# Kernel tuning notes

Hardware: AMD Instinct MI355X
Metric: run time of the kernel (lower is better)

## Reference

```python
import jax, jax.numpy as jnp
import numpy as np

B, N, D = 1024, 100000, 512


def setup_inputs() -> dict:
    key = jax.random.key(0)
    k1, k2, k3 = jax.random.split(key, 3)
    x_t = jax.random.normal(k1, (B, D), dtype=jnp.float32)
    # keep t away from 0/1 so b_t = 1 - t is well conditioned
    t = jax.random.uniform(k2, (B,), dtype=jnp.float32, minval=0.05, maxval=0.95)
    dataset = jax.random.normal(k3, (N, D), dtype=jnp.float32)
    return {"x_t": x_t, "t": t, "dataset": dataset}


def reference(x_t, t, dataset):
    # Straight-line AffineInterp: a_t = t, b_t = 1 - t, dot_a = 1, dot_b = -1.
    # Original detaches coeffs (detach=True).
    a_t = jax.lax.stop_gradient(t)
    b_t = jax.lax.stop_gradient(1.0 - t)
    dot_a_t = jnp.ones_like(a_t)
    dot_b_t = -jnp.ones_like(b_t)

    dataset_norm = jnp.sum(dataset * dataset, axis=1)          # (N,)
    term_1 = jnp.sum(x_t * x_t, axis=1)                        # (B,)
    term_2 = jnp.einsum('bd,nd->bn', x_t, dataset)             # (B, N)

    # ||x_t - a_t * x1||^2 expanded, scaled by -1/(2 b_t^2)
    logit = (term_1[:, None]
             - 2.0 * a_t[:, None] * term_2
             + (a_t * a_t)[:, None] * dataset_norm[None, :])
    logit = (-1.0 / (2.0 * b_t * b_t))[:, None] * logit        # (B, N)

    prob = jax.nn.softmax(logit, axis=1)                       # (B, N)
    data_coeff = dot_a_t - a_t * dot_b_t / b_t                 # (B,)
    prob = prob * data_coeff[:, None]

    weighted_dataset = jnp.einsum('bn,nd->bd', prob, dataset)  # (B, D)
    v = (dot_b_t / b_t)[:, None] * x_t + weighted_dataset
    return v
```

## Files before the change

### kernel.cpp

```cpp
#include <hip/hip_runtime.h>
#include <math.h>

#define B_SZ 1024
#define N_SZ 100000
#define D_SZ 512
#define NBLK 3125

typedef __attribute__((ext_vector_type(8))) short short8;
typedef __attribute__((ext_vector_type(16))) float float16;

__device__ __forceinline__ unsigned f2bf(float x) {
    unsigned u = __float_as_uint(x);
    u += 0x7FFFu + ((u >> 16) & 1u);
    return u >> 16;
}
__device__ __forceinline__ float bf2f(unsigned h) {
    return __uint_as_float(h << 16);
}

__global__ __launch_bounds__(256) void pre_kernel(
    const float* __restrict__ ds, const float* __restrict__ x_t,
    short* __restrict__ Yh, short* __restrict__ Yl, short* __restrict__ Yt,
    short* __restrict__ Xh, short* __restrict__ Xl, float* __restrict__ norms)
{
    __shared__ unsigned short YS[32 * 512];
    const int bx = blockIdx.x, tid = threadIdx.x;
    if (bx < NBLK) {
        const int row = tid >> 3, seg = tid & 7;
        const size_t g = (size_t)(bx * 32 + row) * 512 + seg * 64;
        const int ls = row * 512 + seg * 64;
        float nrm = 0.f;
        #pragma unroll
        for (int i = 0; i < 16; i++) {
            float4 v = *(const float4*)(ds + g + i * 4);
            nrm += v.x*v.x + v.y*v.y + v.z*v.z + v.w*v.w;
            unsigned h0 = f2bf(v.x), h1 = f2bf(v.y), h2 = f2bf(v.z), h3 = f2bf(v.w);
            unsigned l0 = f2bf(v.x - bf2f(h0)), l1 = f2bf(v.y - bf2f(h1));
            unsigned l2 = f2bf(v.z - bf2f(h2)), l3 = f2bf(v.w - bf2f(h3));
            uint2 hw = make_uint2(h0 | (h1 << 16), h2 | (h3 << 16));
            uint2 lw = make_uint2(l0 | (l1 << 16), l2 | (l3 << 16));
            *(uint2*)(Yh + g + i * 4) = hw;
            *(uint2*)(Yl + g + i * 4) = lw;
            *(uint2*)(YS + ls + i * 4) = hw;
        }
        nrm += __shfl_xor(nrm, 1, 64);
        nrm += __shfl_xor(nrm, 2, 64);
        nrm += __shfl_xor(nrm, 4, 64);
        if ((tid & 7) == 0) norms[bx * 32 + row] = nrm;
        __syncthreads();
        #pragma unroll
        for (int r = 0; r < 2; r++) {
            const int d = tid + r * 256;
            unsigned w[16];
            #pragma unroll
            for (int j = 0; j < 16; j++) {
                unsigned lo = YS[(2 * j) * 512 + d];
                unsigned hi = YS[(2 * j + 1) * 512 + d];
                w[j] = lo | (hi << 16);
            }
            uint4* dst = (uint4*)(Yt + (size_t)bx * 16384 + d * 32);
            dst[0] = make_uint4(w[0], w[1], w[2], w[3]);
            dst[1] = make_uint4(w[4], w[5], w[6], w[7]);
            dst[2] = make_uint4(w[8], w[9], w[10], w[11]);
            dst[3] = make_uint4(w[12], w[13], w[14], w[15]);
        }
    } else {
        const int xb = bx - NBLK;
        #pragma unroll
        for (int k = 0; k < 16; k++) {
            const size_t i4 = (size_t)xb * 4096 + k * 256 + tid;
            float4 v = *(const float4*)(x_t + i4 * 4);
            unsigned h0 = f2bf(v.x), h1 = f2bf(v.y), h2 = f2bf(v.z), h3 = f2bf(v.w);
            unsigned l0 = f2bf(v.x - bf2f(h0)), l1 = f2bf(v.y - bf2f(h1));
            unsigned l2 = f2bf(v.z - bf2f(h2)), l3 = f2bf(v.w - bf2f(h3));
            *(uint2*)(Xh + i4 * 4) = make_uint2(h0 | (h1 << 16), h2 | (h3 << 16));
            *(uint2*)(Xl + i4 * 4) = make_uint2(l0 | (l1 << 16), l2 | (l3 << 16));
        }
    }
}

__global__ __launch_bounds__(512, 2) void attn_kernel(
    const float* __restrict__ t,
    const short* __restrict__ Xh, const short* __restrict__ Xl,
    const short* __restrict__ Yh, const short* __restrict__ Yl,
    const short* __restrict__ Yt, const float* __restrict__ norms,
    float* __restrict__ m_part, float* __restrict__ l_part,
    float* __restrict__ acc_part, int chunk)
{
    __shared__ short YhL[2 * 32 * 512];
    __shared__ float slots[4 * 64 * 33];
    __shared__ float Pbuf[64 * 36];
    __shared__ float c1A[64], c2A[64], mAs[64], lAs[64], alA[64];
    __shared__ float nrmL[32];

    const int tid = threadIdx.x;
    const int wave = tid >> 6, lane = tid & 63;
    const int half = lane >> 5, l31 = lane & 31;

    int qbi = blockIdx.x, si = blockIdx.y;
    if (gridDim.x == 16 && (gridDim.y & 7) == 0) {
        int g = gridDim.y >> 3;
        int fid = blockIdx.x + blockIdx.y * 16;
        int xcd = fid & 7, j = fid >> 3;
        si = xcd + 8 * (j % g);
        qbi = j / g;
    }
    const int qb = qbi * 64;
    const int s = si;
    const int n0s = s * chunk;
    const int n1 = min(N_SZ, n0s + chunk);
    const int numTiles = (n1 - n0s + 31) >> 5;

    if (tid < 64) {
        float tv = t[qb + tid];
        float bt = 1.0f - tv;
        float i2 = 1.0f / (2.0f * bt * bt);
        c1A[tid] = 2.0f * tv * i2;
        c2A[tid] = tv * tv * i2;
        mAs[tid] = -1e30f;
        lAs[tid] = 0.0f;
        alA[tid] = 0.0f;
    }

    if (wave < 4) {
        short8 XF[2][8][2];
        #pragma unroll
        for (int qt = 0; qt < 2; qt++)
            #pragma unroll
            for (int kc = 0; kc < 8; kc++) {
                size_t off = (size_t)(qb + qt * 32 + l31) * 512 + wave * 128 + kc * 16 + half * 8;
                XF[qt][kc][0] = *(const short8*)(Xh + off);
                XF[qt][kc][1] = *(const short8*)(Xl + off);
            }
        {
            #pragma unroll
            for (int j = 0; j < 8; j++) {
                int r = wave * 8 + j;
                const int gsw = (lane * 8) ^ ((r & 7) << 3);
                const short* gh = Yh + (size_t)(n0s + r) * 512 + gsw;
                __builtin_amdgcn_global_load_lds(
                    (const __attribute__((address_space(1))) unsigned int*)gh,
                    (__attribute__((address_space(3))) unsigned int*)&YhL[r * 512], 16, 0, 0);
            }
        }
        __syncthreads();

        for (int it = 0; it <= numTiles; ++it) {
            short8 ALf[8];
            if (it < numTiles) {
                const int n0 = n0s + it * 32;
                const short* ylrow = Yl + (size_t)(n0 + l31) * 512 + wave * 128 + half * 8;
                #pragma unroll
                for (int kc = 0; kc < 8; kc++)
                    ALf[kc] = *(const short8*)(ylrow + kc * 16);
                if (wave == 0 && lane < 32) nrmL[lane] = norms[n0 + lane];
            }
            if (it + 1 < numTiles) {
                const int n0n = n0s + (it + 1) * 32;
                short* dstb = YhL + ((it + 1) & 1) * (32 * 512);
                #pragma unroll
                for (int j = 0; j < 8; j++) {
                    int r = wave * 8 + j;
                    const int gsw = (lane * 8) ^ ((r & 7) << 3);
                    const short* gh = Yh + (size_t)(n0n + r) * 512 + gsw;
                    __builtin_amdgcn_global_load_lds(
                        (const __attribute__((address_space(1))) unsigned int*)gh,
                        (__attribute__((address_space(3))) unsigned int*)&dstb[r * 512], 16, 0, 0);
                }
            }
            if (it < numTiles) {
                const short* Yb = YhL + (it & 1) * (32 * 512);
                float16 S0, S1;
                #pragma unroll
                for (int e = 0; e < 16; e++) { S0[e] = 0.f; S1[e] = 0.f; }
                #pragma unroll
                for (int kc = 0; kc < 8; kc++) {
                    const int koff = wave * 128 + kc * 16 + half * 8;
                    const int ksw = koff ^ ((l31 & 7) << 3);
                    short8 Ah = *(const short8*)(Yb + l31 * 512 + ksw);
                    S0 = __builtin_amdgcn_mfma_f32_32x32x16_bf16(Ah, XF[0][kc][0], S0, 0, 0, 0);
                    S0 = __builtin_amdgcn_mfma_f32_32x32x16_bf16(Ah, XF[0][kc][1], S0, 0, 0, 0);
                    S0 = __builtin_amdgcn_mfma_f32_32x32x16_bf16(ALf[kc], XF[0][kc][0], S0, 0, 0, 0);
                    S1 = __builtin_amdgcn_mfma_f32_32x32x16_bf16(Ah, XF[1][kc][0], S1, 0, 0, 0);
                    S1 = __builtin_amdgcn_mfma_f32_32x32x16_bf16(Ah, XF[1][kc][1], S1, 0, 0, 0);
                    S1 = __builtin_amdgcn_mfma_f32_32x32x16_bf16(ALf[kc], XF[1][kc][0], S1, 0, 0, 0);
                }
                float* sb = &slots[wave * 2112];
                #pragma unroll
                for (int qt = 0; qt < 2; qt++) {
                    float* rowp = sb + (qt * 32 + l31) * 33;
                    #pragma unroll
                    for (int r = 0; r < 16; r++) {
                        int n = (r & 3) + 8 * (r >> 2) + 4 * half;
                        rowp[n] = qt ? S1[r] : S0[r];
                    }
                }
            }
            __syncthreads();

            if (it < numTiles) {
                int ql = lane >> 2, nq = lane & 3;
                int q = wave * 16 + ql;
                float c1q = c1A[q], c2q = c2A[q];
                float lg[8];
                float mt = -1e30f;
                #pragma unroll
                for (int j = 0; j < 8; j++) {
                    int n = nq * 8 + j;
                    float dd = slots[q * 33 + n] + slots[2112 + q * 33 + n]
                             + slots[4224 + q * 33 + n] + slots[6336 + q * 33 + n];
                    lg[j] = c1q * dd - c2q * nrmL[n];
                    mt = fmaxf(mt, lg[j]);
                }
                mt = fmaxf(mt, __shfl_xor(mt, 1, 64));
                mt = fmaxf(mt, __shfl_xor(mt, 2, 64));
                float mo = mAs[q];
                float mn = fmaxf(mo, mt);
                float al = __expf(mo - mn);
                float ls = 0.f;
                #pragma unroll
                for (int j = 0; j < 8; j++) {
                    float p = __expf(lg[j] - mn);
                    Pbuf[q * 36 + nq * 8 + j] = p;
                    ls += p;
                }
                ls += __shfl_xor(ls, 1, 64);
                ls += __shfl_xor(ls, 2, 64);
                if (nq == 0) {
                    mAs[q] = mn;
                    lAs[q] = lAs[q] * al + ls;
                    alA[q] = al;
                }
            }
            __syncthreads();
        }
        if (tid < 64) {
            m_part[(size_t)s * B_SZ + qb + tid] = mAs[tid];
            l_part[(size_t)s * B_SZ + qb + tid] = lAs[tid];
        }
    } else {
        const int dbase = (wave - 4) * 128;
        float16 O[4][2];
        #pragma unroll
        for (int dt = 0; dt < 4; dt++)
            #pragma unroll
            for (int qt = 0; qt < 2; qt++)
                #pragma unroll
                for (int e = 0; e < 16; e++) O[dt][qt][e] = 0.f;

        __syncthreads();

        for (int it = 0; it <= numTiles; ++it) {
            if (it > 0) {
                int blk = (n0s + (it - 1) * 32) >> 5;
                const short* yb = Yt + (size_t)blk * 16384;
                short8 AF[4][2];
                #pragma unroll
                for (int dt = 0; dt < 4; dt++)
                    #pragma unroll
                    for (int kc = 0; kc < 2; kc++)
                        AF[dt][kc] = *(const short8*)(yb + (dbase + dt * 32 + l31) * 32 + kc * 16 + half * 8);
                float al0 = alA[l31], al1 = alA[32 + l31];
                #pragma unroll
                for (int dt = 0; dt < 4; dt++) {
                    O[dt][0] *= al0;
                    O[dt][1] *= al1;
                }
                short8 BF[2][2];
                #pragma unroll
                for (int qt = 0; qt < 2; qt++)
                    #pragma unroll
                    for (int kc = 0; kc < 2; kc++) {
                        const float* pr = &Pbuf[(qt * 32 + l31) * 36 + kc * 16 + half * 8];
                        float4 pa = *(const float4*)pr;
                        float4 pb = *(const float4*)(pr + 4);
                        short8 b;
                        b[0] = (short)f2bf(pa.x); b[1] = (short)f2bf(pa.y);
                        b[2] = (short)f2bf(pa.z); b[3] = (short)f2bf(pa.w);
                        b[4] = (short)f2bf(pb.x); b[5] = (short)f2bf(pb.y);
                        b[6] = (short)f2bf(pb.z); b[7] = (short)f2bf(pb.w);
                        BF[qt][kc] = b;
                    }
                #pragma unroll
                for (int dt = 0; dt < 4; dt++)
                    #pragma unroll
                    for (int qt = 0; qt < 2; qt++)
                        #pragma unroll
                        for (int kc = 0; kc < 2; kc++)
                            O[dt][qt] = __builtin_amdgcn_mfma_f32_32x32x16_bf16(
                                AF[dt][kc], BF[qt][kc], O[dt][qt], 0, 0, 0);
            }
            __syncthreads();
            __syncthreads();
        }
        #pragma unroll
        for (int dt = 0; dt < 4; dt++)
            #pragma unroll
            for (int qt = 0; qt < 2; qt++) {
                int q = qb + qt * 32 + l31;
                float* op = acc_part + ((size_t)s * B_SZ + q) * D_SZ + dbase + dt * 32 + 4 * half;
                #pragma unroll
                for (int rg = 0; rg < 4; rg++) {
                    float4 v = make_float4(O[dt][qt][4 * rg], O[dt][qt][4 * rg + 1],
                                           O[dt][qt][4 * rg + 2], O[dt][qt][4 * rg + 3]);
                    *(float4*)(op + 8 * rg) = v;
                }
            }
    }
}

__global__ __launch_bounds__(256) void combine_kernel(
    const float* __restrict__ x_t, const float* __restrict__ t,
    const float* __restrict__ m_part, const float* __restrict__ l_part,
    const float* __restrict__ acc_part, float* __restrict__ out, int nsplit)
{
    int q = blockIdx.x;
    int tid = threadIdx.x;
    float M = -1e30f;
    for (int s = 0; s < nsplit; s++) M = fmaxf(M, m_part[(size_t)s * B_SZ + q]);
    float L = 0.f;
    for (int s = 0; s < nsplit; s++)
        L += l_part[(size_t)s * B_SZ + q] * __expf(m_part[(size_t)s * B_SZ + q] - M);

    float tv = t[q];
    float bt = 1.0f - tv;
    float coeff = 1.0f + tv / bt;
    float invb = 1.0f / bt;
    float invL = 1.0f / L;

    int d = tid * 2;
    float2 w = make_float2(0.f, 0.f);
    for (int s = 0; s < nsplit; s++) {
        float sc = __expf(m_part[(size_t)s * B_SZ + q] - M);
        float2 av = *(const float2*)(acc_part + ((size_t)s * B_SZ + q) * D_SZ + d);
        w.x += sc * av.x; w.y += sc * av.y;
    }
    float2 xv = *(const float2*)(x_t + (size_t)q * D_SZ + d);
    float2 o;
    o.x = -invb * xv.x + coeff * w.x * invL;
    o.y = -invb * xv.y + coeff * w.y * invL;
    *(float2*)(out + (size_t)q * D_SZ + d) = o;
}

extern "C" void kernel_launch(void* const* d_in, const int* in_sizes, int n_in,
                              void* d_out, int out_size, void* d_ws, size_t ws_size,
                              hipStream_t stream) {
    const float* x_t = (const float*)d_in[0];
    const float* t   = (const float*)d_in[1];
    const float* ds  = (const float*)d_in[2];
    float* out = (float*)d_out;

    short* wsS = (short*)d_ws;
    short* Yh = wsS;
    short* Yl = wsS + 51200000;
    short* Yt = wsS + 102400000;
    short* Xh = wsS + 153600000;
    short* Xl = wsS + 154124288;
    float* fbase = (float*)((char*)d_ws + 309297152);
    float* norms = fbase;
    int nsplit = 16;
    while (nsplit > 1 &&
           309697152ULL + (size_t)nsplit * 1024 * 4 * (2 + 512) > ws_size)
        nsplit >>= 1;
    float* m_part = fbase + 100000;
    float* l_part = m_part + (size_t)nsplit * B_SZ;
    float* acc    = l_part + (size_t)nsplit * B_SZ;
    int chunk = 32 * ((N_SZ + 32 * nsplit - 1) / (32 * nsplit));

    pre_kernel<<<dim3(NBLK + 32), dim3(256), 0, stream>>>(ds, x_t, Yh, Yl, Yt, Xh, Xl, norms);
    attn_kernel<<<dim3(16, nsplit), dim3(512), 0, stream>>>(
        t, Xh, Xl, Yh, Yl, Yt, norms, m_part, l_part, acc, chunk);
    combine_kernel<<<dim3(B_SZ), dim3(256), 0, stream>>>(
        x_t, t, m_part, l_part, acc, out, nsplit);
}
```

Before: 1.218 ms.

## Stage low-bf16 dataset tile through LDS and split MFMA accumulator chains

```diff
diff --git a/kernel.cpp b/kernel.cpp
--- a/kernel.cpp
+++ b/kernel.cpp
@@ -88,6 +88,7 @@
     float* __restrict__ acc_part, int chunk)
 {
     __shared__ short YhL[2 * 32 * 512];
+    __shared__ short YlL[32 * 512];
     __shared__ float slots[4 * 64 * 33];
     __shared__ float Pbuf[64 * 36];
     __shared__ float c1A[64], c2A[64], mAs[64], lAs[64], alA[64];
@@ -132,29 +133,22 @@
                 XF[qt][kc][0] = *(const short8*)(Xh + off);
                 XF[qt][kc][1] = *(const short8*)(Xl + off);
             }
-        {
-            #pragma unroll
-            for (int j = 0; j < 8; j++) {
-                int r = wave * 8 + j;
-                const int gsw = (lane * 8) ^ ((r & 7) << 3);
-                const short* gh = Yh + (size_t)(n0s + r) * 512 + gsw;
-                __builtin_amdgcn_global_load_lds(
-                    (const __attribute__((address_space(1))) unsigned int*)gh,
-                    (__attribute__((address_space(3))) unsigned int*)&YhL[r * 512], 16, 0, 0);
-            }
+        #pragma unroll
+        for (int j = 0; j < 8; j++) {
+            int r = wave * 8 + j;
+            const int gsw = (lane * 8) ^ ((r & 7) << 3);
+            const short* gh = Yh + (size_t)(n0s + r) * 512 + gsw;
+            const short* gl = Yl + (size_t)(n0s + r) * 512 + gsw;
+            __builtin_amdgcn_global_load_lds(
+                (const __attribute__((address_space(1))) unsigned int*)gh,
+                (__attribute__((address_space(3))) unsigned int*)&YhL[r * 512], 16, 0, 0);
+            __builtin_amdgcn_global_load_lds(
+                (const __attribute__((address_space(1))) unsigned int*)gl,
+                (__attribute__((address_space(3))) unsigned int*)&YlL[r * 512], 16, 0, 0);
         }
         __syncthreads();
 
         for (int it = 0; it <= numTiles; ++it) {
-            short8 ALf[8];
-            if (it < numTiles) {
-                const int n0 = n0s + it * 32;
-                const short* ylrow = Yl + (size_t)(n0 + l31) * 512 + wave * 128 + half * 8;
-                #pragma unroll
-                for (int kc = 0; kc < 8; kc++)
-                    ALf[kc] = *(const short8*)(ylrow + kc * 16);
-                if (wave == 0 && lane < 32) nrmL[lane] = norms[n0 + lane];
-            }
             if (it + 1 < numTiles) {
                 const int n0n = n0s + (it + 1) * 32;
                 short* dstb = YhL + ((it + 1) & 1) * (32 * 512);
@@ -169,22 +163,29 @@
                 }
             }
             if (it < numTiles) {
+                if (wave == 0 && lane < 32) nrmL[lane] = norms[n0s + it * 32 + lane];
                 const short* Yb = YhL + (it & 1) * (32 * 512);
-                float16 S0, S1;
-                #pragma unroll
-                for (int e = 0; e < 16; e++) { S0[e] = 0.f; S1[e] = 0.f; }
+                float16 S0a, S0b, S0c, S1a, S1b, S1c;
+                #pragma unroll
+                for (int e = 0; e < 16; e++) {
+                    S0a[e] = 0.f; S0b[e] = 0.f; S0c[e] = 0.f;
+                    S1a[e] = 0.f; S1b[e] = 0.f; S1c[e] = 0.f;
+                }
+                __builtin_amdgcn_s_setprio(1);
                 #pragma unroll
                 for (int kc = 0; kc < 8; kc++) {
                     const int koff = wave * 128 + kc * 16 + half * 8;
                     const int ksw = koff ^ ((l31 & 7) << 3);
                     short8 Ah = *(const short8*)(Yb + l31 * 512 + ksw);
-                    S0 = __builtin_amdgcn_mfma_f32_32x32x16_bf16(Ah, XF[0][kc][0], S0, 0, 0, 0);
-                    S0 = __builtin_amdgcn_mfma_f32_32x32x16_bf16(Ah, XF[0][kc][1], S0, 0, 0, 0);
-                    S0 = __builtin_amdgcn_mfma_f32_32x32x16_bf16(ALf[kc], XF[0][kc][0], S0, 0, 0, 0);
-                    S1 = __builtin_amdgcn_mfma_f32_32x32x16_bf16(Ah, XF[1][kc][0], S1, 0, 0, 0);
-                    S1 = __builtin_amdgcn_mfma_f32_32x32x16_bf16(Ah, XF[1][kc][1], S1, 0, 0, 0);
-                    S1 = __builtin_amdgcn_mfma_f32_32x32x16_bf16(ALf[kc], XF[1][kc][0], S1, 0, 0, 0);
-                }
+                    short8 Al = *(const short8*)(YlL + l31 * 512 + ksw);
+                    S0a = __builtin_amdgcn_mfma_f32_32x32x16_bf16(Ah, XF[0][kc][0], S0a, 0, 0, 0);
+                    S0b = __builtin_amdgcn_mfma_f32_32x32x16_bf16(Ah, XF[0][kc][1], S0b, 0, 0, 0);
+                    S0c = __builtin_amdgcn_mfma_f32_32x32x16_bf16(Al, XF[0][kc][0], S0c, 0, 0, 0);
+                    S1a = __builtin_amdgcn_mfma_f32_32x32x16_bf16(Ah, XF[1][kc][0], S1a, 0, 0, 0);
+                    S1b = __builtin_amdgcn_mfma_f32_32x32x16_bf16(Ah, XF[1][kc][1], S1b, 0, 0, 0);
+                    S1c = __builtin_amdgcn_mfma_f32_32x32x16_bf16(Al, XF[1][kc][0], S1c, 0, 0, 0);
+                }
+                __builtin_amdgcn_s_setprio(0);
                 float* sb = &slots[wave * 2112];
                 #pragma unroll
                 for (int qt = 0; qt < 2; qt++) {
@@ -192,12 +193,26 @@
                     #pragma unroll
                     for (int r = 0; r < 16; r++) {
                         int n = (r & 3) + 8 * (r >> 2) + 4 * half;
-                        rowp[n] = qt ? S1[r] : S0[r];
+                        float v = qt ? (S1a[r] + S1b[r] + S1c[r])
+                                     : (S0a[r] + S0b[r] + S0c[r]);
+                        rowp[n] = v;
                     }
                 }
             }
             __syncthreads();
 
+            if (it + 1 < numTiles) {
+                const int n0n = n0s + (it + 1) * 32;
+                #pragma unroll
+                for (int j = 0; j < 8; j++) {
+                    int r = wave * 8 + j;
+                    const int gsw = (lane * 8) ^ ((r & 7) << 3);
+                    const short* gl = Yl + (size_t)(n0n + r) * 512 + gsw;
+                    __builtin_amdgcn_global_load_lds(
+                        (const __attribute__((address_space(1))) unsigned int*)gl,
+                        (__attribute__((address_space(3))) unsigned int*)&YlL[r * 512], 16, 0, 0);
+                }
+            }
             if (it < numTiles) {
                 int ql = lane >> 2, nq = lane & 3;
                 int q = wave * 16 + ql;
```

New measurement: 1.382 ms. +13.5%, slower.

## Single-buffer Yh tile, split MFMA accumulators, store probabilities as bf16

Applied to the files above, without the earlier changes.

```diff
diff --git a/kernel.cpp b/kernel.cpp
--- a/kernel.cpp
+++ b/kernel.cpp
@@ -87,9 +87,9 @@
     float* __restrict__ m_part, float* __restrict__ l_part,
     float* __restrict__ acc_part, int chunk)
 {
-    __shared__ short YhL[2 * 32 * 512];
+    __shared__ short YhL[32 * 512];
     __shared__ float slots[4 * 64 * 33];
-    __shared__ float Pbuf[64 * 36];
+    __shared__ short PbufH[64 * 40];
     __shared__ float c1A[64], c2A[64], mAs[64], lAs[64], alA[64];
     __shared__ float nrmL[32];
 
@@ -132,32 +132,61 @@
                 XF[qt][kc][0] = *(const short8*)(Xh + off);
                 XF[qt][kc][1] = *(const short8*)(Xl + off);
             }
-        {
-            #pragma unroll
-            for (int j = 0; j < 8; j++) {
-                int r = wave * 8 + j;
-                const int gsw = (lane * 8) ^ ((r & 7) << 3);
-                const short* gh = Yh + (size_t)(n0s + r) * 512 + gsw;
-                __builtin_amdgcn_global_load_lds(
-                    (const __attribute__((address_space(1))) unsigned int*)gh,
-                    (__attribute__((address_space(3))) unsigned int*)&YhL[r * 512], 16, 0, 0);
-            }
+        #pragma unroll
+        for (int j = 0; j < 8; j++) {
+            int r = wave * 8 + j;
+            const int gsw = (lane * 8) ^ ((r & 7) << 3);
+            const short* gh = Yh + (size_t)(n0s + r) * 512 + gsw;
+            __builtin_amdgcn_global_load_lds(
+                (const __attribute__((address_space(1))) unsigned int*)gh,
+                (__attribute__((address_space(3))) unsigned int*)&YhL[r * 512], 16, 0, 0);
         }
         __syncthreads();
 
         for (int it = 0; it <= numTiles; ++it) {
-            short8 ALf[8];
             if (it < numTiles) {
                 const int n0 = n0s + it * 32;
+                if (wave == 0 && lane < 32) nrmL[lane] = norms[n0 + lane];
+                short8 AL[8];
                 const short* ylrow = Yl + (size_t)(n0 + l31) * 512 + wave * 128 + half * 8;
                 #pragma unroll
                 for (int kc = 0; kc < 8; kc++)
-                    ALf[kc] = *(const short8*)(ylrow + kc * 16);
-                if (wave == 0 && lane < 32) nrmL[lane] = norms[n0 + lane];
-            }
+                    AL[kc] = *(const short8*)(ylrow + kc * 16);
+                asm volatile("" ::: "memory");
+                float16 S0a, S0b, S1a, S1b;
+                #pragma unroll
+                for (int e = 0; e < 16; e++) {
+                    S0a[e] = 0.f; S0b[e] = 0.f; S1a[e] = 0.f; S1b[e] = 0.f;
+                }
+                #pragma unroll
+                for (int kc = 0; kc < 8; kc++) {
+                    const int ksw = (wave * 128 + kc * 16 + half * 8) ^ ((l31 & 7) << 3);
+                    short8 Ah = *(const short8*)(YhL + l31 * 512 + ksw);
+                    S0a = __builtin_amdgcn_mfma_f32_32x32x16_bf16(Ah, XF[0][kc][0], S0a, 0, 0, 0);
+                    S0b = __builtin_amdgcn_mfma_f32_32x32x16_bf16(Ah, XF[0][kc][1], S0b, 0, 0, 0);
+                    S1a = __builtin_amdgcn_mfma_f32_32x32x16_bf16(Ah, XF[1][kc][0], S1a, 0, 0, 0);
+                    S1b = __builtin_amdgcn_mfma_f32_32x32x16_bf16(Ah, XF[1][kc][1], S1b, 0, 0, 0);
+                }
+                #pragma unroll
+                for (int kc = 0; kc < 8; kc++) {
+                    S0a = __builtin_amdgcn_mfma_f32_32x32x16_bf16(AL[kc], XF[0][kc][0], S0a, 0, 0, 0);
+                    S1a = __builtin_amdgcn_mfma_f32_32x32x16_bf16(AL[kc], XF[1][kc][0], S1a, 0, 0, 0);
+                }
+                float* sb = &slots[wave * 2112];
+                #pragma unroll
+                for (int qt = 0; qt < 2; qt++) {
+                    float* rowp = sb + (qt * 32 + l31) * 33;
+                    #pragma unroll
+                    for (int r = 0; r < 16; r++) {
+                        int n = (r & 3) + 8 * (r >> 2) + 4 * half;
+                        rowp[n] = qt ? (S1a[r] + S1b[r]) : (S0a[r] + S0b[r]);
+                    }
+                }
+            }
+            __syncthreads();
+
             if (it + 1 < numTiles) {
                 const int n0n = n0s + (it + 1) * 32;
-                short* dstb = YhL + ((it + 1) & 1) * (32 * 512);
                 #pragma unroll
                 for (int j = 0; j < 8; j++) {
                     int r = wave * 8 + j;
@@ -165,39 +194,9 @@
                     const short* gh = Yh + (size_t)(n0n + r) * 512 + gsw;
                     __builtin_amdgcn_global_load_lds(
                         (const __attribute__((address_space(1))) unsigned int*)gh,
-                        (__attribute__((address_space(3))) unsigned int*)&dstb[r * 512], 16, 0, 0);
-                }
-            }
-            if (it < numTiles) {
-                const short* Yb = YhL + (it & 1) * (32 * 512);
-                float16 S0, S1;
-                #pragma unroll
-                for (int e = 0; e < 16; e++) { S0[e] = 0.f; S1[e] = 0.f; }
-                #pragma unroll
-                for (int kc = 0; kc < 8; kc++) {
-                    const int koff = wave * 128 + kc * 16 + half * 8;
-                    const int ksw = koff ^ ((l31 & 7) << 3);
-                    short8 Ah = *(const short8*)(Yb + l31 * 512 + ksw);
-                    S0 = __builtin_amdgcn_mfma_f32_32x32x16_bf16(Ah, XF[0][kc][0], S0, 0, 0, 0);
-                    S0 = __builtin_amdgcn_mfma_f32_32x32x16_bf16(Ah, XF[0][kc][1], S0, 0, 0, 0);
-                    S0 = __builtin_amdgcn_mfma_f32_32x32x16_bf16(ALf[kc], XF[0][kc][0], S0, 0, 0, 0);
-                    S1 = __builtin_amdgcn_mfma_f32_32x32x16_bf16(Ah, XF[1][kc][0], S1, 0, 0, 0);
-                    S1 = __builtin_amdgcn_mfma_f32_32x32x16_bf16(Ah, XF[1][kc][1], S1, 0, 0, 0);
-                    S1 = __builtin_amdgcn_mfma_f32_32x32x16_bf16(ALf[kc], XF[1][kc][0], S1, 0, 0, 0);
-                }
-                float* sb = &slots[wave * 2112];
-                #pragma unroll
-                for (int qt = 0; qt < 2; qt++) {
-                    float* rowp = sb + (qt * 32 + l31) * 33;
-                    #pragma unroll
-                    for (int r = 0; r < 16; r++) {
-                        int n = (r & 3) + 8 * (r >> 2) + 4 * half;
-                        rowp[n] = qt ? S1[r] : S0[r];
-                    }
-                }
-            }
-            __syncthreads();
-
+                        (__attribute__((address_space(3))) unsigned int*)&YhL[r * 512], 16, 0, 0);
+                }
+            }
             if (it < numTiles) {
                 int ql = lane >> 2, nq = lane & 3;
                 int q = wave * 16 + ql;
@@ -218,12 +217,15 @@
                 float mn = fmaxf(mo, mt);
                 float al = __expf(mo - mn);
                 float ls = 0.f;
-                #pragma unroll
-                for (int j = 0; j < 8; j++) {
-                    float p = __expf(lg[j] - mn);
-                    Pbuf[q * 36 + nq * 8 + j] = p;
-                    ls += p;
-                }
+                unsigned wpk[4];
+                #pragma unroll
+                for (int j = 0; j < 4; j++) {
+                    float p0 = __expf(lg[2 * j] - mn);
+                    float p1 = __expf(lg[2 * j + 1] - mn);
+                    ls += p0 + p1;
+                    wpk[j] = f2bf(p0) | (f2bf(p1) << 16);
+                }
+                *(uint4*)(&PbufH[q * 40 + nq * 8]) = make_uint4(wpk[0], wpk[1], wpk[2], wpk[3]);
                 ls += __shfl_xor(ls, 1, 64);
                 ls += __shfl_xor(ls, 2, 64);
                 if (nq == 0) {
@@ -270,17 +272,8 @@
                 #pragma unroll
                 for (int qt = 0; qt < 2; qt++)
                     #pragma unroll
-                    for (int kc = 0; kc < 2; kc++) {
-                        const float* pr = &Pbuf[(qt * 32 + l31) * 36 + kc * 16 + half * 8];
-                        float4 pa = *(const float4*)pr;
-                        float4 pb = *(const float4*)(pr + 4);
-                        short8 b;
-                        b[0] = (short)f2bf(pa.x); b[1] = (short)f2bf(pa.y);
-                        b[2] = (short)f2bf(pa.z); b[3] = (short)f2bf(pa.w);
-                        b[4] = (short)f2bf(pb.x); b[5] = (short)f2bf(pb.y);
-                        b[6] = (short)f2bf(pb.z); b[7] = (short)f2bf(pb.w);
-                        BF[qt][kc] = b;
-                    }
+                    for (int kc = 0; kc < 2; kc++)
+                        BF[qt][kc] = *(const short8*)(&PbufH[(qt * 32 + l31) * 40 + kc * 16 + half * 8]);
                 #pragma unroll
                 for (int dt = 0; dt < 4; dt++)
                     #pragma unroll
```

Result: slower. 1.244 ms (+2.1%).
